# Performance work log

Measured on AMD Instinct MI355X. Metric: run time of the kernel, lower is better.

## Reference

```python
import jax, jax.numpy as jnp
import numpy as np
from jax import lax

KS, STRIDE, DIL, PAD = 3, 1, 1, 1
B, C_IN, C_OUT, D = 1, 16, 16, 64
K = KS ** 3


def setup_inputs():
    key = jax.random.key(0)
    k1, k2, k3 = jax.random.split(key, 3)
    x = jax.random.normal(k1, (B, C_IN, D, D, D), jnp.float32)
    std = 1.0 / float(np.sqrt(C_IN * K))
    kernel = jax.random.uniform(k2, (K, C_IN, C_OUT), jnp.float32, -std, std)
    # module zero-inits pkernel; use small random values so interp path is exercised
    pkernel = jax.random.normal(k3, (K, C_IN, 3 * K), jnp.float32) * 0.01
    return {"x": x, "kernel": kernel, "pkernel": pkernel}


def _deform_conv3d(x, kernel, pkernel):
    Bn, C, Dd, H, W = x.shape
    Kt = kernel.shape[0]
    # offset-predicting conv: pkernel [K, C_in, 3K] -> conv weight [3K, C_in, kd, kh, kw]
    w_off = jnp.transpose(pkernel.reshape(KS, KS, KS, C, 3 * Kt), (4, 3, 0, 1, 2))
    off = lax.conv_general_dilated(
        x, w_off, (STRIDE,) * 3, [(PAD, PAD)] * 3,
        rhs_dilation=(DIL,) * 3,
        dimension_numbers=("NCDHW", "OIDHW", "NCDHW"))
    Do, Ho, Wo = off.shape[2], off.shape[3], off.shape[4]
    off = off.reshape(Bn, Kt, 3, Do, Ho, Wo)  # 3 offset coords per kernel tap

    # base sampling grid: out_pos*stride - pad + tap*dilation, then add predicted offset
    r = jnp.arange(KS)
    tap = jnp.stack(jnp.meshgrid(r, r, r, indexing="ij"), -1).reshape(Kt, 3) * DIL - PAD
    gz = (jnp.arange(Do) * STRIDE).astype(x.dtype)
    gy = (jnp.arange(Ho) * STRIDE).astype(x.dtype)
    gx = (jnp.arange(Wo) * STRIDE).astype(x.dtype)
    cz = gz[None, None, :, None, None] + tap[None, :, 0, None, None, None] + off[:, :, 0]
    cy = gy[None, None, None, :, None] + tap[None, :, 1, None, None, None] + off[:, :, 1]
    cx = gx[None, None, None, None, :] + tap[None, :, 2, None, None, None] + off[:, :, 2]

    x_flat = x.reshape(Bn, C, Dd * H * W)

    def gather(idx):  # idx [B,K,Do,Ho,Wo] int32 -> [B,C,K,Do,Ho,Wo]
        g = jax.vmap(lambda xf, ix: xf[:, ix.reshape(-1)])(x_flat, idx)
        return g.reshape(Bn, C, Kt, Do, Ho, Wo)

    z0f = jnp.floor(cz); y0f = jnp.floor(cy); x0f = jnp.floor(cx)
    fz, fy, fx = cz - z0f, cy - y0f, cx - x0f
    z0 = z0f.astype(jnp.int32); y0 = y0f.astype(jnp.int32); x0 = x0f.astype(jnp.int32)

    # trilinear interp: accumulate 8 corners (zero outside volume)
    acc = jnp.zeros((Bn, C, Kt, Do, Ho, Wo), x.dtype)
    for dz in (0, 1):
        for dy in (0, 1):
            for dx in (0, 1):
                zi, yi, xi = z0 + dz, y0 + dy, x0 + dx
                valid = ((zi >= 0) & (zi < Dd) & (yi >= 0) & (yi < H)
                         & (xi >= 0) & (xi < W)).astype(x.dtype)
                w = ((fz if dz else 1.0 - fz) * (fy if dy else 1.0 - fy)
                     * (fx if dx else 1.0 - fx)) * valid
                idx = (jnp.clip(zi, 0, Dd - 1) * (H * W)
                       + jnp.clip(yi, 0, H - 1) * W + jnp.clip(xi, 0, W - 1))
                acc = acc + gather(idx) * w[:, None]

    # weighted sum over taps: kernel [K, C_in, C_out]
    return jnp.einsum("bckdhw,kco->bodhw", acc, kernel)


def reference(x, kernel, pkernel):
    return _deform_conv3d(x, kernel, pkernel)
```

## Files before the change

kernel.cpp:

```cpp
#include <hip/hip_runtime.h>

#define D 64
#define DD 4096
#define DDD 262144
#define K 27

typedef __bf16  bf16x8 __attribute__((ext_vector_type(8)));
typedef float   f32x4  __attribute__((ext_vector_type(4)));
typedef float   f32x2  __attribute__((ext_vector_type(2)));
typedef float   f32x16 __attribute__((ext_vector_type(16)));
typedef unsigned int u32x4 __attribute__((ext_vector_type(4)));

#define HX 12
#define HY 8
#define HZ 6
#define HROW 12
#define HPLN 96
#define HSP  576
#define CPAD 24

#define WSW_CH (14*6*64)
#define KSW_CH (27*64)
#define KSW_OFF 88064

__global__ __launch_bounds__(256) void prep_weights(const float* __restrict__ pk,
                                                    const float* __restrict__ kern,
                                                    __bf16* __restrict__ Wsw,
                                                    __bf16* __restrict__ Ksw) {
    int t = blockIdx.x * 256 + threadIdx.x;
    if (t < WSW_CH) {
        int lane = t & 63;
        int sm = t >> 6;
        int s = sm / 6, mt = sm - 6 * s;
        int m = mt * 16 + (lane & 15);
        int q = lane >> 4;
        bf16x8 w;
#pragma unroll
        for (int j = 0; j < 8; ++j) {
            int k = 32 * s + 8 * q + j;
            int kt = k >> 4, c = k & 15;
            float wv = (kt < K && m < 81) ? pk[kt * 1296 + c * 81 + m] : 0.0f;
            w[j] = (__bf16)wv;
        }
        *(bf16x8*)(Wsw + t * 8) = w;
    } else if (t < WSW_CH + KSW_CH) {
        int u = t - WSW_CH;
        int kt = u >> 6, lane = u & 63;
        int m = lane & 31, kh = lane >> 5;
        bf16x8 w;
#pragma unroll
        for (int j = 0; j < 8; ++j) {
            int c = kh * 8 + j;
            float wv = (m < 16) ? kern[kt * 256 + c * 16 + m] : 0.0f;
            w[j] = (__bf16)wv;
        }
        *(bf16x8*)(Ksw + u * 8) = w;
    }
}

__global__ __launch_bounds__(256, 3) void deform_main(
    const float* __restrict__ x,
    const __bf16* __restrict__ Wsw,
    const __bf16* __restrict__ Ksw,
    float* __restrict__ out)
{
    __shared__ __bf16 s_h[HSP * CPAD];
    __shared__ __bf16 s_off[81 * 64];
    __shared__ __bf16 s_v[4 * 1024];

    const int tid  = threadIdx.x;
    const int lane = tid & 63;
    const int wave = __builtin_amdgcn_readfirstlane(tid >> 6);

    const int bx0 = blockIdx.x * 8;
    const int by0 = blockIdx.y * 4;
    const int bz0 = blockIdx.z * 2;

    for (int i = tid; i < HSP; i += 256) {
        int z = i / HPLN;
        int r = i - z * HPLN;
        int y = r / HROW;
        int xx = r - y * HROW;
        int gz = bz0 - 2 + z, gy = by0 - 2 + y, gx = bx0 - 2 + xx;
        bool in = (unsigned)gz < D && (unsigned)gy < D && (unsigned)gx < D;
        bf16x8 a = {}, b = {};
        if (in) {
            const float* p = x + (gz * DD + gy * D + gx);
#pragma unroll
            for (int c = 0; c < 8; ++c) a[c] = (__bf16)p[c * DDD];
#pragma unroll
            for (int c = 0; c < 8; ++c) b[c] = (__bf16)p[(c + 8) * DDD];
        }
        *(bf16x8*)(s_h + i * CPAD)     = a;
        *(bf16x8*)(s_h + i * CPAD + 8) = b;
    }
    __syncthreads();

    {
        const int n = lane & 15, q = lane >> 4;
        const int vtz = wave >> 1;
        const int vty = 2 * (wave & 1) + (n >> 3);
        const int vtx = n & 7;
        f32x4 acc[6] = {};
        for (int s = 0; s < 14; ++s) {
            int kt = 2 * s + (q >> 1);
            int ktc = (kt < K) ? kt : 0;
            int kd = ktc / 9, kh = (ktc / 3) % 3, kw = ktc % 3;
            int idx = (vtz + kd + 1) * HPLN + (vty + kh + 1) * HROW + (vtx + kw + 1);
            bf16x8 bfrag = *(const bf16x8*)(s_h + idx * CPAD + (q & 1) * 8);
#pragma unroll
            for (int mt = 0; mt < 6; ++mt) {
                bf16x8 afrag = *(const bf16x8*)(Wsw + ((s * 6 + mt) * 64 + lane) * 8);
                acc[mt] = __builtin_amdgcn_mfma_f32_16x16x32_bf16(afrag, bfrag, acc[mt], 0, 0, 0);
            }
        }
        const int v = wave * 16 + n;
#pragma unroll
        for (int mt = 0; mt < 6; ++mt)
#pragma unroll
            for (int r = 0; r < 4; ++r) {
                int o = mt * 16 + q * 4 + r;
                if (o < 81) s_off[o * 64 + v] = (__bf16)acc[mt][r];
            }
    }
    __syncthreads();

    const int tx = lane & 7, ty = (lane >> 3) & 3, tz = lane >> 5;
    const int gz = bz0 + tz, gy = by0 + ty, gx = bx0 + tx;
    const int l31 = lane & 31, lh = lane >> 5;
    __bf16* sv = s_v + wave * 1024;

    f32x16 acc2[2] = {};

    const int ntaps = (wave < 3) ? 7 : 6;
    for (int t = 0; t < ntaps; ++t) {
        const int kt = wave * 7 + t;
        const int kd = kt / 9, kh = (kt / 3) % 3, kw = kt % 3;
        float cz = (float)(gz + kd - 1) + (float)s_off[(3 * kt + 0) * 64 + lane];
        float cy = (float)(gy + kh - 1) + (float)s_off[(3 * kt + 1) * 64 + lane];
        float cx = (float)(gx + kw - 1) + (float)s_off[(3 * kt + 2) * 64 + lane];
        float zf = floorf(cz), yf = floorf(cy), xf = floorf(cx);
        float fz = cz - zf, fy = cy - yf, fx = cx - xf;
        int z0 = (int)zf, y0 = (int)yf, x0 = (int)xf;
        int hz0 = z0 - bz0 + 2, hy0 = y0 - by0 + 2, hx0 = x0 - bx0 + 2;

        f32x2 val[8] = {};
        if ((unsigned)hz0 < (unsigned)(HZ - 1) && (unsigned)hy0 < (unsigned)(HY - 1)
            && (unsigned)hx0 < (unsigned)(HX - 1)) {
#pragma unroll
            for (int dz = 0; dz < 2; ++dz) {
                float wz = dz ? fz : 1.0f - fz;
#pragma unroll
                for (int dy = 0; dy < 2; ++dy) {
                    float wzy = wz * (dy ? fy : 1.0f - fy);
#pragma unroll
                    for (int dx = 0; dx < 2; ++dx) {
                        float w = wzy * (dx ? fx : 1.0f - fx);
                        int idx = (hz0 + dz) * HPLN + (hy0 + dy) * HROW + (hx0 + dx);
                        bf16x8 c0 = *(const bf16x8*)(s_h + idx * CPAD);
                        bf16x8 c1 = *(const bf16x8*)(s_h + idx * CPAD + 8);
                        u32x4 u0 = __builtin_bit_cast(u32x4, c0);
                        u32x4 u1 = __builtin_bit_cast(u32x4, c1);
                        f32x2 w2 = {w, w};
#pragma unroll
                        for (int d = 0; d < 4; ++d) {
                            unsigned int u = u0[d];
                            f32x2 h;
                            h.x = __builtin_bit_cast(float, u << 16);
                            h.y = __builtin_bit_cast(float, u & 0xffff0000u);
                            val[d] += w2 * h;
                        }
#pragma unroll
                        for (int d = 0; d < 4; ++d) {
                            unsigned int u = u1[d];
                            f32x2 h;
                            h.x = __builtin_bit_cast(float, u << 16);
                            h.y = __builtin_bit_cast(float, u & 0xffff0000u);
                            val[d + 4] += w2 * h;
                        }
                    }
                }
            }
        } else {
#pragma unroll
            for (int dz = 0; dz < 2; ++dz) {
                int zi = z0 + dz;
                float wz = dz ? fz : 1.0f - fz;
#pragma unroll
                for (int dy = 0; dy < 2; ++dy) {
                    int yi = y0 + dy;
                    float wzy = wz * (dy ? fy : 1.0f - fy);
#pragma unroll
                    for (int dx = 0; dx < 2; ++dx) {
                        int xi = x0 + dx;
                        if ((unsigned)zi < D && (unsigned)yi < D && (unsigned)xi < D) {
                            float w = wzy * (dx ? fx : 1.0f - fx);
                            int base = zi * DD + yi * D + xi;
#pragma unroll
                            for (int c = 0; c < 16; ++c)
                                val[c >> 1][c & 1] += w * x[c * DDD + base];
                        }
                    }
                }
            }
        }

        bf16x8 v0, v1;
#pragma unroll
        for (int d = 0; d < 4; ++d) { v0[2*d] = (__bf16)val[d].x;   v0[2*d+1] = (__bf16)val[d].y; }
#pragma unroll
        for (int d = 0; d < 4; ++d) { v1[2*d] = (__bf16)val[d+4].x; v1[2*d+1] = (__bf16)val[d+4].y; }
        *(bf16x8*)(sv + lane * 16)     = v0;
        *(bf16x8*)(sv + lane * 16 + 8) = v1;
        asm volatile("s_waitcnt lgkmcnt(0)" ::: "memory");

        bf16x8 af = *(const bf16x8*)(Ksw + (kt * 64 + lane) * 8);
        bf16x8 b0 = *(const bf16x8*)(sv + l31 * 16 + lh * 8);
        acc2[0] = __builtin_amdgcn_mfma_f32_32x32x16_bf16(af, b0, acc2[0], 0, 0, 0);
        bf16x8 b1 = *(const bf16x8*)(sv + (32 + l31) * 16 + lh * 8);
        acc2[1] = __builtin_amdgcn_mfma_f32_32x32x16_bf16(af, b1, acc2[1], 0, 0, 0);
        asm volatile("" ::: "memory");
    }

    __syncthreads();
    float* s_red = (float*)s_h;
#pragma unroll
    for (int g = 0; g < 2; ++g)
#pragma unroll
        for (int r = 0; r < 8; ++r) {
            int o = (r & 3) + 8 * (r >> 2) + 4 * lh;
            s_red[(wave * 64 + g * 32 + l31) * 17 + o] = acc2[g][r];
        }
    __syncthreads();

#pragma unroll
    for (int j = 0; j < 4; ++j) {
        int o = wave * 4 + j;
        float s = s_red[(0 * 64 + lane) * 17 + o]
                + s_red[(1 * 64 + lane) * 17 + o]
                + s_red[(2 * 64 + lane) * 17 + o]
                + s_red[(3 * 64 + lane) * 17 + o];
        out[o * DDD + gz * DD + gy * D + gx] = s;
    }
}

extern "C" void kernel_launch(void* const* d_in, const int* in_sizes, int n_in,
                              void* d_out, int out_size, void* d_ws, size_t ws_size,
                              hipStream_t stream) {
    const float* x    = (const float*)d_in[0];
    const float* kern = (const float*)d_in[1];
    const float* pk   = (const float*)d_in[2];
    float* out = (float*)d_out;

    __bf16* Wsw = (__bf16*)d_ws;
    __bf16* Ksw = (__bf16*)((char*)d_ws + KSW_OFF);

    prep_weights<<<28, 256, 0, stream>>>(pk, kern, Wsw, Ksw);
    deform_main<<<dim3(8, 16, 32), 256, 0, stream>>>(x, Wsw, Ksw, out);
}
```

Before: 173.8 us.

## Switch to fp16 storage and packed half-precision trilinear interpolation

```diff
diff --git a/kernel.cpp b/kernel.cpp
--- a/kernel.cpp
+++ b/kernel.cpp
@@ -5,11 +5,11 @@
 #define DDD 262144
 #define K 27
 
-typedef __bf16  bf16x8 __attribute__((ext_vector_type(8)));
-typedef float   f32x4  __attribute__((ext_vector_type(4)));
-typedef float   f32x2  __attribute__((ext_vector_type(2)));
-typedef float   f32x16 __attribute__((ext_vector_type(16)));
-typedef unsigned int u32x4 __attribute__((ext_vector_type(4)));
+typedef _Float16 half8  __attribute__((ext_vector_type(8)));
+typedef _Float16 half2v __attribute__((ext_vector_type(2)));
+typedef float    f32x4  __attribute__((ext_vector_type(4)));
+typedef float    f32x2  __attribute__((ext_vector_type(2)));
+typedef float    f32x16 __attribute__((ext_vector_type(16)));
 
 #define HX 12
 #define HY 8
@@ -18,15 +18,20 @@
 #define HPLN 96
 #define HSP  576
 #define CPAD 24
+#define VSLOT 24
 
 #define WSW_CH (14*6*64)
 #define KSW_CH (27*64)
 #define KSW_OFF 88064
 
+__device__ inline half2v h2of(half8 v, int d) {
+    half2v r; r.x = v[2*d]; r.y = v[2*d+1]; return r;
+}
+
 __global__ __launch_bounds__(256) void prep_weights(const float* __restrict__ pk,
                                                     const float* __restrict__ kern,
-                                                    __bf16* __restrict__ Wsw,
-                                                    __bf16* __restrict__ Ksw) {
+                                                    _Float16* __restrict__ Wsw,
+                                                    _Float16* __restrict__ Ksw) {
     int t = blockIdx.x * 256 + threadIdx.x;
     if (t < WSW_CH) {
         int lane = t & 63;
@@ -34,39 +39,39 @@
         int s = sm / 6, mt = sm - 6 * s;
         int m = mt * 16 + (lane & 15);
         int q = lane >> 4;
-        bf16x8 w;
+        half8 w;
 #pragma unroll
         for (int j = 0; j < 8; ++j) {
             int k = 32 * s + 8 * q + j;
             int kt = k >> 4, c = k & 15;
             float wv = (kt < K && m < 81) ? pk[kt * 1296 + c * 81 + m] : 0.0f;
-            w[j] = (__bf16)wv;
-        }
-        *(bf16x8*)(Wsw + t * 8) = w;
+            w[j] = (_Float16)wv;
+        }
+        *(half8*)(Wsw + t * 8) = w;
     } else if (t < WSW_CH + KSW_CH) {
         int u = t - WSW_CH;
         int kt = u >> 6, lane = u & 63;
         int m = lane & 31, kh = lane >> 5;
-        bf16x8 w;
+        half8 w;
 #pragma unroll
         for (int j = 0; j < 8; ++j) {
             int c = kh * 8 + j;
             float wv = (m < 16) ? kern[kt * 256 + c * 16 + m] : 0.0f;
-            w[j] = (__bf16)wv;
-        }
-        *(bf16x8*)(Ksw + u * 8) = w;
+            w[j] = (_Float16)wv;
+        }
+        *(half8*)(Ksw + u * 8) = w;
     }
 }
 
 __global__ __launch_bounds__(256, 3) void deform_main(
     const float* __restrict__ x,
-    const __bf16* __restrict__ Wsw,
-    const __bf16* __restrict__ Ksw,
+    const _Float16* __restrict__ Wsw,
+    const _Float16* __restrict__ Ksw,
     float* __restrict__ out)
 {
-    __shared__ __bf16 s_h[HSP * CPAD];
-    __shared__ __bf16 s_off[81 * 64];
-    __shared__ __bf16 s_v[4 * 1024];
+    __shared__ _Float16 s_h[HSP * CPAD];
+    __shared__ _Float16 s_off[81 * 64];
+    __shared__ _Float16 s_v[4 * 64 * VSLOT];
 
     const int tid  = threadIdx.x;
     const int lane = tid & 63;
@@ -83,16 +88,16 @@
         int xx = r - y * HROW;
         int gz = bz0 - 2 + z, gy = by0 - 2 + y, gx = bx0 - 2 + xx;
         bool in = (unsigned)gz < D && (unsigned)gy < D && (unsigned)gx < D;
-        bf16x8 a = {}, b = {};
+        half8 a = {}, b = {};
         if (in) {
             const float* p = x + (gz * DD + gy * D + gx);
 #pragma unroll
-            for (int c = 0; c < 8; ++c) a[c] = (__bf16)p[c * DDD];
-#pragma unroll
-            for (int c = 0; c < 8; ++c) b[c] = (__bf16)p[(c + 8) * DDD];
-        }
-        *(bf16x8*)(s_h + i * CPAD)     = a;
-        *(bf16x8*)(s_h + i * CPAD + 8) = b;
+            for (int c = 0; c < 8; ++c) a[c] = (_Float16)p[c * DDD];
+#pragma unroll
+            for (int c = 0; c < 8; ++c) b[c] = (_Float16)p[(c + 8) * DDD];
+        }
+        *(half8*)(s_h + i * CPAD)     = a;
+        *(half8*)(s_h + i * CPAD + 8) = b;
     }
     __syncthreads();
 
@@ -107,11 +112,11 @@
             int ktc = (kt < K) ? kt : 0;
             int kd = ktc / 9, kh = (ktc / 3) % 3, kw = ktc % 3;
             int idx = (vtz + kd + 1) * HPLN + (vty + kh + 1) * HROW + (vtx + kw + 1);
-            bf16x8 bfrag = *(const bf16x8*)(s_h + idx * CPAD + (q & 1) * 8);
+            half8 bfrag = *(const half8*)(s_h + idx * CPAD + (q & 1) * 8);
 #pragma unroll
             for (int mt = 0; mt < 6; ++mt) {
-                bf16x8 afrag = *(const bf16x8*)(Wsw + ((s * 6 + mt) * 64 + lane) * 8);
-                acc[mt] = __builtin_amdgcn_mfma_f32_16x16x32_bf16(afrag, bfrag, acc[mt], 0, 0, 0);
+                half8 afrag = *(const half8*)(Wsw + ((s * 6 + mt) * 64 + lane) * 8);
+                acc[mt] = __builtin_amdgcn_mfma_f32_16x16x32_f16(afrag, bfrag, acc[mt], 0, 0, 0);
             }
         }
         const int v = wave * 16 + n;
@@ -120,7 +125,7 @@
 #pragma unroll
             for (int r = 0; r < 4; ++r) {
                 int o = mt * 16 + q * 4 + r;
-                if (o < 81) s_off[o * 64 + v] = (__bf16)acc[mt][r];
+                if (o < 81) s_off[o * 64 + v] = (_Float16)acc[mt][r];
             }
     }
     __syncthreads();
@@ -128,7 +133,7 @@
     const int tx = lane & 7, ty = (lane >> 3) & 3, tz = lane >> 5;
     const int gz = bz0 + tz, gy = by0 + ty, gx = bx0 + tx;
     const int l31 = lane & 31, lh = lane >> 5;
-    __bf16* sv = s_v + wave * 1024;
+    _Float16* sv = s_v + wave * 64 * VSLOT;
 
     f32x16 acc2[2] = {};
 
@@ -144,7 +149,7 @@
         int z0 = (int)zf, y0 = (int)yf, x0 = (int)xf;
         int hz0 = z0 - bz0 + 2, hy0 = y0 - by0 + 2, hx0 = x0 - bx0 + 2;
 
-        f32x2 val[8] = {};
+        half2v val2[8] = {};
         if ((unsigned)hz0 < (unsigned)(HZ - 1) && (unsigned)hy0 < (unsigned)(HY - 1)
             && (unsigned)hx0 < (unsigned)(HX - 1)) {
 #pragma unroll
@@ -157,31 +162,21 @@
                     for (int dx = 0; dx < 2; ++dx) {
                         float w = wzy * (dx ? fx : 1.0f - fx);
                         int idx = (hz0 + dz) * HPLN + (hy0 + dy) * HROW + (hx0 + dx);
-                        bf16x8 c0 = *(const bf16x8*)(s_h + idx * CPAD);
-                        bf16x8 c1 = *(const bf16x8*)(s_h + idx * CPAD + 8);
-                        u32x4 u0 = __builtin_bit_cast(u32x4, c0);
-                        u32x4 u1 = __builtin_bit_cast(u32x4, c1);
-                        f32x2 w2 = {w, w};
-#pragma unroll
-                        for (int d = 0; d < 4; ++d) {
-                            unsigned int u = u0[d];
-                            f32x2 h;
-                            h.x = __builtin_bit_cast(float, u << 16);
-                            h.y = __builtin_bit_cast(float, u & 0xffff0000u);
-                            val[d] += w2 * h;
-                        }
-#pragma unroll
-                        for (int d = 0; d < 4; ++d) {
-                            unsigned int u = u1[d];
-                            f32x2 h;
-                            h.x = __builtin_bit_cast(float, u << 16);
-                            h.y = __builtin_bit_cast(float, u & 0xffff0000u);
-                            val[d + 4] += w2 * h;
-                        }
+                        half8 c0 = *(const half8*)(s_h + idx * CPAD);
+                        half8 c1 = *(const half8*)(s_h + idx * CPAD + 8);
+                        _Float16 wh = (_Float16)w;
+                        half2v w2; w2.x = wh; w2.y = wh;
+#pragma unroll
+                        for (int d = 0; d < 4; ++d)
+                            val2[d] += w2 * h2of(c0, d);
+#pragma unroll
+                        for (int d = 0; d < 4; ++d)
+                            val2[d + 4] += w2 * h2of(c1, d);
                     }
                 }
             }
         } else {
+            f32x2 valf[8] = {};
 #pragma unroll
             for (int dz = 0; dz < 2; ++dz) {
                 int zi = z0 + dz;
@@ -198,27 +193,32 @@
                             int base = zi * DD + yi * D + xi;
 #pragma unroll
                             for (int c = 0; c < 16; ++c)
-                                val[c >> 1][c & 1] += w * x[c * DDD + base];
+                                valf[c >> 1][c & 1] += w * x[c * DDD + base];
                         }
                     }
                 }
             }
-        }
-
-        bf16x8 v0, v1;
-#pragma unroll
-        for (int d = 0; d < 4; ++d) { v0[2*d] = (__bf16)val[d].x;   v0[2*d+1] = (__bf16)val[d].y; }
-#pragma unroll
-        for (int d = 0; d < 4; ++d) { v1[2*d] = (__bf16)val[d+4].x; v1[2*d+1] = (__bf16)val[d+4].y; }
-        *(bf16x8*)(sv + lane * 16)     = v0;
-        *(bf16x8*)(sv + lane * 16 + 8) = v1;
+#pragma unroll
+            for (int d = 0; d < 8; ++d) {
+                val2[d].x = (_Float16)valf[d].x;
+                val2[d].y = (_Float16)valf[d].y;
+            }
+        }
+
+        half8 v0, v1;
+#pragma unroll
+        for (int d = 0; d < 4; ++d) { v0[2*d] = val2[d].x;     v0[2*d+1] = val2[d].y; }
+#pragma unroll
+        for (int d = 0; d < 4; ++d) { v1[2*d] = val2[d+4].x;   v1[2*d+1] = val2[d+4].y; }
+        *(half8*)(sv + lane * VSLOT)     = v0;
+        *(half8*)(sv + lane * VSLOT + 8) = v1;
         asm volatile("s_waitcnt lgkmcnt(0)" ::: "memory");
 
-        bf16x8 af = *(const bf16x8*)(Ksw + (kt * 64 + lane) * 8);
-        bf16x8 b0 = *(const bf16x8*)(sv + l31 * 16 + lh * 8);
-        acc2[0] = __builtin_amdgcn_mfma_f32_32x32x16_bf16(af, b0, acc2[0], 0, 0, 0);
-        bf16x8 b1 = *(const bf16x8*)(sv + (32 + l31) * 16 + lh * 8);
-        acc2[1] = __builtin_amdgcn_mfma_f32_32x32x16_bf16(af, b1, acc2[1], 0, 0, 0);
+        half8 af = *(const half8*)(Ksw + (kt * 64 + lane) * 8);
+        half8 b0 = *(const half8*)(sv + l31 * VSLOT + lh * 8);
+        acc2[0] = __builtin_amdgcn_mfma_f32_32x32x16_f16(af, b0, acc2[0], 0, 0, 0);
+        half8 b1 = *(const half8*)(sv + (32 + l31) * VSLOT + lh * 8);
+        acc2[1] = __builtin_amdgcn_mfma_f32_32x32x16_f16(af, b1, acc2[1], 0, 0, 0);
         asm volatile("" ::: "memory");
     }
 
@@ -252,8 +252,8 @@
     const float* pk   = (const float*)d_in[2];
     float* out = (float*)d_out;
 
-    __bf16* Wsw = (__bf16*)d_ws;
-    __bf16* Ksw = (__bf16*)((char*)d_ws + KSW_OFF);
+    _Float16* Wsw = (_Float16*)d_ws;
+    _Float16* Ksw = (_Float16*)((char*)d_ws + KSW_OFF);
 
     prep_weights<<<28, 256, 0, stream>>>(pk, kern, Wsw, Ksw);
     deform_main<<<dim3(8, 16, 32), 256, 0, stream>>>(x, Wsw, Ksw, out);
```

Result: no change. 176.3 us (+1.4%).
